# Performance work log

Measured on AMD Instinct MI355X. Metric: run time of the kernel, lower is better.

The kernel has to match this reference:

```python
import jax, jax.numpy as jnp
import numpy as np

B, T, S, N, C, H = 2, 16, 256, 32, 3072, 24
D = C // H  # 128 head_dim
EPS = 1e-6


def _layernorm(x):
    # LayerNorm, elementwise_affine=False, eps=1e-6
    mu = jnp.mean(x, axis=-1, keepdims=True)
    var = jnp.mean(jnp.square(x - mu), axis=-1, keepdims=True)
    return (x - mu) * jax.lax.rsqrt(var + EPS)


def _rmsnorm(x, w):
    # RMSNorm with learnable weight, computed in fp32 (matches x.float() path)
    ms = jnp.mean(jnp.square(x), axis=-1, keepdims=True)
    return x * jax.lax.rsqrt(ms + EPS) * w


def setup_inputs() -> dict:
    key = jax.random.key(0)
    ks = jax.random.split(key, 8)
    f = lambda k, sh: jax.random.normal(k, sh, dtype=jnp.float32)
    sc = 1.0 / np.sqrt(C)
    return {
        "x": f(ks[0], (B, T * S, C)),
        "motion_vec": f(ks[1], (B, T, N, C)),
        "motion_mask": jax.random.uniform(ks[2], (B, T * S), dtype=jnp.float32),
        "w_kv": f(ks[3], (2 * C, C)) * sc,
        "b_kv": jnp.zeros((2 * C,), jnp.float32),
        "w_q": f(ks[4], (C, C)) * sc,
        "b_q": jnp.zeros((C,), jnp.float32),
        "w_o": f(ks[5], (C, C)) * sc,
        "b_o": jnp.zeros((C,), jnp.float32),
        "q_norm_w": jnp.ones((D,), jnp.float32),
        "k_norm_w": jnp.ones((D,), jnp.float32),
    }


def reference(x, motion_vec, motion_mask, w_kv, b_kv, w_q, b_q, w_o, b_o,
              q_norm_w, k_norm_w):
    x_motion = _layernorm(motion_vec)            # [B,T,N,C]
    x_feat = _layernorm(x)                       # [B,T*S,C]

    kv = x_motion @ w_kv.T + b_kv                # [B,T,N,2C]
    kv = kv.reshape(B, T, N, 2, H, D)
    k, v = kv[:, :, :, 0], kv[:, :, :, 1]        # [B,T,N,H,D]

    q = (x_feat @ w_q.T + b_q).reshape(B, T, S, H, D)
    q = _rmsnorm(q, q_norm_w)
    k = _rmsnorm(k, k_norm_w)

    # frame-local cross-attention: queries = spatial tokens, keys = motion tokens
    scale = 1.0 / jnp.sqrt(jnp.float32(D))
    scores = jnp.einsum('btshd,btnhd->bthsn', q, k) * scale  # [B,T,H,S,N]
    probs = jax.nn.softmax(scores, axis=-1)
    attn = jnp.einsum('bthsn,btnhd->btshd', probs, v)        # [B,T,S,H,D]
    attn = attn.reshape(B, T * S, C)

    out = attn @ w_o.T + b_o                     # [B,T*S,C]
    return out * motion_mask[:, :, None]
```

## Files before the change

kernel.cpp:

```cpp
#include <hip/hip_runtime.h>
#include <math.h>

typedef unsigned short u16;
typedef unsigned int u32;
typedef short bf16x8 __attribute__((ext_vector_type(8)));
typedef float f32x4 __attribute__((ext_vector_type(4)));
typedef u16 u16x4 __attribute__((ext_vector_type(4)));
typedef u16 u16x8 __attribute__((ext_vector_type(8)));
typedef u32 u32x4 __attribute__((ext_vector_type(4)));

static __device__ __forceinline__ float b2f(u16 u) {
  union { u32 i; float f; } v; v.i = ((u32)u) << 16; return v.f;
}
static __device__ __forceinline__ u16 f2b(float f) {
  union { float f; u32 i; } v; v.f = f;
  u32 r = v.i + 0x7fffu + ((v.i >> 16) & 1u);
  return (u16)(r >> 16);
}
static __device__ __forceinline__ void cvt16(const float* src, u16* dst, int i) {
  f32x4 v = *(const f32x4*)(src + (size_t)i * 4);
  u16x4 w; w.x = f2b(v.x); w.y = f2b(v.y); w.z = f2b(v.z); w.w = f2b(v.w);
  *(u16x4*)(dst + (size_t)i * 4) = w;
}

static __device__ __forceinline__ void g2l16(const void* g, void* l) {
  typedef __attribute__((address_space(1))) const void gvoid;
  typedef __attribute__((address_space(3))) void lvoid;
  __builtin_amdgcn_global_load_lds((gvoid*)g, (lvoid*)l, 16, 0, 0);
}

__global__ __launch_bounds__(256)
void wcvt_kernel(const float* __restrict__ src, u16* __restrict__ dst, int n4)
{
  for (int i = blockIdx.x * 256 + threadIdx.x; i < n4; i += gridDim.x * 256)
    cvt16(src, dst, i);
}

__global__ __launch_bounds__(256)
void prep_kernel(const float* __restrict__ x, const float* __restrict__ mv,
                 u16* __restrict__ xf, u16* __restrict__ xm,
                 const float* __restrict__ wq, u16* __restrict__ wqs,
                 const float* __restrict__ wkv, u16* __restrict__ wkvs)
{
  const int b = blockIdx.x, tid = threadIdx.x;
  if (b >= 9216) {
    if (b < 10240) {
      const int n4 = 3072 * 3072 / 4;
      for (int i = (b - 9216) * 256 + tid; i < n4; i += 1024 * 256) cvt16(wq, wqs, i);
    } else {
      const int n4 = 6144 * 3072 / 4;
      for (int i = (b - 10240) * 256 + tid; i < n4; i += 1024 * 256) cvt16(wkv, wkvs, i);
    }
    return;
  }
  const float* src; u16* dst;
  if (b < 8192) { src = x + (size_t)b * 3072;          dst = xf + (size_t)b * 3072; }
  else          { src = mv + (size_t)(b - 8192) * 3072; dst = xm + (size_t)(b - 8192) * 3072; }

  f32x4 vals[3];
  #pragma unroll
  for (int i = 0; i < 3; ++i) vals[i] = *(const f32x4*)(src + tid * 4 + i * 1024);

  float s1 = 0.f, s2 = 0.f;
  #pragma unroll
  for (int i = 0; i < 3; ++i) {
    f32x4 v = vals[i];
    s1 += v.x + v.y + v.z + v.w;
    s2 += v.x * v.x + v.y * v.y + v.z * v.z + v.w * v.w;
  }
  #pragma unroll
  for (int o = 32; o > 0; o >>= 1) { s1 += __shfl_down(s1, o); s2 += __shfl_down(s2, o); }
  __shared__ float r1[4], r2[4];
  const int wv = tid >> 6, ln = tid & 63;
  if (ln == 0) { r1[wv] = s1; r2[wv] = s2; }
  __syncthreads();
  const float t1 = r1[0] + r1[1] + r1[2] + r1[3];
  const float t2 = r2[0] + r2[1] + r2[2] + r2[3];
  const float mu = t1 * (1.f / 3072.f);
  const float rs = rsqrtf(t2 * (1.f / 3072.f) - mu * mu + 1e-6f);
  #pragma unroll
  for (int i = 0; i < 3; ++i) {
    f32x4 v = vals[i]; u16x4 w;
    w.x = f2b((v.x - mu) * rs); w.y = f2b((v.y - mu) * rs);
    w.z = f2b((v.z - mu) * rs); w.w = f2b((v.w - mu) * rs);
    *(u16x4*)(dst + tid * 4 + i * 1024) = w;
  }
}

template<int EPI, typename TOUT>
__global__ __launch_bounds__(512, 1)
void gemm8p(const u16* __restrict__ A, const u16* __restrict__ Wb,
            const float* __restrict__ bias, const float* __restrict__ mask,
            TOUT* __restrict__ C, int M, int N, int K)
{
  __shared__ __align__(16) u16 L[65536];
  const int tid = threadIdx.x, wave = tid >> 6, lane = tid & 63;
  const int wr = wave >> 2, wc = wave & 3;
  const int lr = lane & 15, lg = lane >> 4;

  const int nwg = gridDim.x;
  const int bid = (blockIdx.x & 7) * (nwg >> 3) + (blockIdx.x >> 3);
  const int nbx = N >> 8;
  const int brow = (bid / nbx) << 8;
  const int bcol = (bid % nbx) << 8;

  const u16* gA = A + (size_t)brow * K;
  const u16* gB = Wb + (size_t)bcol * K;

  const int sr = tid >> 3;
  const int sc = 8 * ((tid & 7) ^ (sr & 7));
  const int ch0 = 8 * (lg ^ (lr & 7));
  const int ch1 = 8 * ((4 + lg) ^ (lr & 7));

  f32x4 acc[8][4] = {};

  auto SG = [&](int sel, int d, int h, int T) {
    const u16* g = (sel == 0 ? gA : gB) + (size_t)(h * 128 + sr) * K + T * 64 + sc;
    u16* l = &L[sel * 32768 + (d * 2 + h) * 8192 + tid * 8];
    g2l16(g, l);
    g2l16(g + (size_t)64 * K, l + 4096);
  };
  auto LDA = [&](int d, int mh, bf16x8 a[4][2]) {
    const u16* base = &L[(d * 2 + wr) * 8192 + mh * 4096 + lr * 64];
    #pragma unroll
    for (int mm = 0; mm < 4; ++mm) {
      a[mm][0] = *(const bf16x8*)&base[mm * 1024 + ch0];
      a[mm][1] = *(const bf16x8*)&base[mm * 1024 + ch1];
    }
  };
  auto LDB = [&](int d, int nh, bf16x8 b[2][2]) {
    const u16* base = &L[32768 + (d * 2 + (wc >> 1)) * 8192 + (wc & 1) * 4096 + nh * 2048 + lr * 64];
    #pragma unroll
    for (int nn = 0; nn < 2; ++nn) {
      b[nn][0] = *(const bf16x8*)&base[nn * 1024 + ch0];
      b[nn][1] = *(const bf16x8*)&base[nn * 1024 + ch1];
    }
  };

#define MM8P(mh, nh, a, b)                                                     \
  __builtin_amdgcn_s_setprio(1);                                               \
  _Pragma("unroll")                                                            \
  for (int mm = 0; mm < 4; ++mm)                                               \
    _Pragma("unroll")                                                          \
    for (int nn = 0; nn < 2; ++nn) {                                           \
      acc[(mh)*4+mm][(nh)*2+nn] = __builtin_amdgcn_mfma_f32_16x16x32_bf16(     \
          a[mm][0], b[nn][0], acc[(mh)*4+mm][(nh)*2+nn], 0, 0, 0);             \
      acc[(mh)*4+mm][(nh)*2+nn] = __builtin_amdgcn_mfma_f32_16x16x32_bf16(     \
          a[mm][1], b[nn][1], acc[(mh)*4+mm][(nh)*2+nn], 0, 0, 0);             \
    }                                                                          \
  __builtin_amdgcn_s_setprio(0);

#define BAR_PRE()                                                              \
  asm volatile("" ::: "memory");                                               \
  __builtin_amdgcn_s_barrier();                                                \
  asm volatile("s_waitcnt lgkmcnt(0)" ::: "memory");                           \
  __builtin_amdgcn_sched_barrier(0);

#define BAR_POST()                                                             \
  asm volatile("" ::: "memory");                                               \
  __builtin_amdgcn_s_barrier();                                                \
  __builtin_amdgcn_sched_barrier(0);

  SG(0, 0, 0, 0); SG(0, 0, 1, 0); SG(1, 0, 0, 0); SG(1, 0, 1, 0);
  SG(0, 1, 0, 1);
  asm volatile("s_waitcnt vmcnt(2)" ::: "memory");
  __builtin_amdgcn_s_barrier();
  __builtin_amdgcn_sched_barrier(0);

  const int NI = K >> 7;
  for (int i = 0; i < NI; ++i) {
    const int t = 2 * i;
    const bool pf = (i + 1) < NI;
    bf16x8 a[4][2], b[2][2];

    LDA(0, 0, a); LDB(0, 0, b);
    SG(0, 1, 1, t + 1);
    BAR_PRE(); MM8P(0, 0, a, b); BAR_POST();

    LDB(0, 1, b);
    SG(1, 1, 0, t + 1);
    BAR_PRE(); MM8P(0, 1, a, b); BAR_POST();

    LDA(0, 1, a);
    SG(1, 1, 1, t + 1);
    BAR_PRE(); MM8P(1, 1, a, b); BAR_POST();

    LDB(0, 0, b);
    if (pf) SG(0, 0, 0, t + 2);
    BAR_PRE(); MM8P(1, 0, a, b);
    if (pf) { asm volatile("s_waitcnt vmcnt(2)" ::: "memory"); }
    else    { asm volatile("s_waitcnt vmcnt(0)" ::: "memory"); }
    BAR_POST();

    LDA(1, 0, a); LDB(1, 0, b);
    if (pf) SG(0, 0, 1, t + 2);
    BAR_PRE(); MM8P(0, 0, a, b); BAR_POST();

    LDB(1, 1, b);
    if (pf) SG(1, 0, 0, t + 2);
    BAR_PRE(); MM8P(0, 1, a, b); BAR_POST();

    LDA(1, 1, a);
    if (pf) SG(1, 0, 1, t + 2);
    BAR_PRE(); MM8P(1, 1, a, b); BAR_POST();

    LDB(1, 0, b);
    if (pf) SG(0, 1, 0, t + 3);
    BAR_PRE(); MM8P(1, 0, a, b);
    if (pf) { asm volatile("s_waitcnt vmcnt(2)" ::: "memory"); }
    BAR_POST();
  }

#undef MM8P
#undef BAR_PRE
#undef BAR_POST

  #pragma unroll
  for (int m = 0; m < 8; ++m) {
    const int row = brow + wr * 128 + m * 16 + (lg << 2);
    #pragma unroll
    for (int n = 0; n < 4; ++n) {
      const int col = bcol + wc * 64 + n * 16 + lr;
      const float bv = bias[col];
      #pragma unroll
      for (int i = 0; i < 4; ++i) {
        float v = acc[m][n][i] + bv;
        if (EPI == 1) v *= mask[row + i];
        if constexpr (__is_same(TOUT, u16))
          C[(size_t)(row + i) * N + col] = f2b(v);
        else
          C[(size_t)(row + i) * N + col] = v;
      }
    }
  }
}

template<int EPI, typename TOUT>
__global__ __launch_bounds__(256, 2)
void gemm256(const u16* __restrict__ A, const u16* __restrict__ Wb,
             const float* __restrict__ bias, const float* __restrict__ mask,
             TOUT* __restrict__ C, int M, int N, int K)
{
  __shared__ __align__(16) u16 L[36864];
  const int tid = threadIdx.x, wave = tid >> 6, lane = tid & 63;

  const int nwg = gridDim.x;
  const int bid = (blockIdx.x & 7) * (nwg >> 3) + (blockIdx.x >> 3);
  const int nbx = N >> 7;
  const int brow = (bid / nbx) << 8;
  const int bcol = (bid % nbx) << 7;
  const int wr = wave >> 1, wc = wave & 1;

  const u16* gA = A + (size_t)brow * K;
  const u16* gB = Wb + (size_t)bcol * K;

  const int srow = tid >> 2;
  const int scol = 8 * ((lane & 3) ^ ((lane >> 3) & 3));
  const int rcoff = 8 * ((lane >> 4) ^ ((lane >> 1) & 3));

  f32x4 acc[8][4] = {};

  auto STAGE = [&](int b, int tk) {
    u16* bufA = &L[b * 12288];
    u16* bufB = bufA + 8192;
    const u16* srcA = gA + tk + scol;
    const u16* srcB = gB + tk + scol;
    #pragma unroll
    for (int j = 0; j < 4; ++j)
      g2l16(srcA + (size_t)(j * 64 + srow) * K, bufA + (j * 64 + wave * 16) * 32);
    #pragma unroll
    for (int j = 0; j < 2; ++j)
      g2l16(srcB + (size_t)(j * 64 + srow) * K, bufB + (j * 64 + wave * 16) * 32);
  };

  auto COMPUTE = [&](int b) {
    const u16* bufA = &L[b * 12288];
    const u16* bufB = bufA + 8192;
    bf16x8 af[8], bfv[4];
    #pragma unroll
    for (int m = 0; m < 8; ++m)
      af[m] = *(const bf16x8*)&bufA[(wr * 128 + m * 16 + (lane & 15)) * 32 + rcoff];
    #pragma unroll
    for (int n = 0; n < 4; ++n)
      bfv[n] = *(const bf16x8*)&bufB[(wc * 64 + n * 16 + (lane & 15)) * 32 + rcoff];
    __builtin_amdgcn_s_setprio(1);
    #pragma unroll
    for (int m = 0; m < 8; ++m)
      #pragma unroll
      for (int n = 0; n < 4; ++n)
        acc[m][n] = __builtin_amdgcn_mfma_f32_16x16x32_bf16(af[m], bfv[n], acc[m][n], 0, 0, 0);
    __builtin_amdgcn_s_setprio(0);
  };

  STAGE(0, 0);
  STAGE(1, 32);
  asm volatile("s_waitcnt vmcnt(6)" ::: "memory");
  __builtin_amdgcn_s_barrier();
  __builtin_amdgcn_sched_barrier(0);

  const int NT = K >> 5;
  int cur = 0;
  for (int t = 0; t < NT; ++t) {
    const bool pf = (t + 2) < NT;
    if (pf) {
      int nb = cur + 2; if (nb >= 3) nb -= 3;
      STAGE(nb, (t + 2) << 5);
    }
    COMPUTE(cur);
    if (pf) asm volatile("s_waitcnt vmcnt(6)" ::: "memory");
    else    asm volatile("s_waitcnt vmcnt(0)" ::: "memory");
    __builtin_amdgcn_s_barrier();
    __builtin_amdgcn_sched_barrier(0);
    if (++cur == 3) cur = 0;
  }

  #pragma unroll
  for (int m = 0; m < 8; ++m) {
    const int row = brow + wr * 128 + m * 16 + ((lane >> 4) << 2);
    #pragma unroll
    for (int n = 0; n < 4; ++n) {
      const int col = bcol + wc * 64 + n * 16 + (lane & 15);
      const float bv = bias[col];
      #pragma unroll
      for (int i = 0; i < 4; ++i) {
        float v = acc[m][n][i] + bv;
        if (EPI == 1) v *= mask[row + i];
        if constexpr (__is_same(TOUT, u16))
          C[(size_t)(row + i) * N + col] = f2b(v);
        else
          C[(size_t)(row + i) * N + col] = v;
      }
    }
  }
}

template<int EPI, typename TOUT>
__global__ __launch_bounds__(256)
void gemm_mixed(const u16* __restrict__ A, const float* __restrict__ W,
                const float* __restrict__ bias, const float* __restrict__ mask,
                TOUT* __restrict__ C, int M, int N, int K)
{
  __shared__ __align__(16) u16 lA[4096];
  __shared__ __align__(16) u16 lB[4096];
  const int tid = threadIdx.x, wave = tid >> 6, lane = tid & 63;
  const int nbx = N >> 7;
  const int brow = (blockIdx.x / nbx) << 7;
  const int bcol = (blockIdx.x % nbx) << 7;
  const int wr = wave >> 1, wc = wave & 1;

  f32x4 acc[4][4] = {};
  const u16* gA = A + (size_t)brow * K;
  const float* gB = W + (size_t)bcol * K;
  const int br = tid >> 1, bk0 = (tid & 1) << 4;
  const float* bsrc0 = gB + (size_t)br * K + bk0;
  u16* bdst = &lB[br * 32 + bk0];

  for (int tk = 0; tk < K; tk += 32) {
    #pragma unroll
    for (int j = 0; j < 2; ++j) {
      const int c = j * 256 + wave * 64 + lane;
      const int r = c >> 2, k8 = (c & 3) << 3;
      g2l16(gA + (size_t)r * K + tk + k8, (char*)lA + (size_t)(j * 256 + wave * 64) * 16);
    }
    {
      const float* src = bsrc0 + tk;
      #pragma unroll
      for (int j = 0; j < 4; ++j) {
        f32x4 v = *(const f32x4*)(src + 4 * j);
        u16x4 w; w.x = f2b(v.x); w.y = f2b(v.y); w.z = f2b(v.z); w.w = f2b(v.w);
        *(u16x4*)(bdst + 4 * j) = w;
      }
    }
    __syncthreads();

    bf16x8 af[4], bfr[4];
    #pragma unroll
    for (int m = 0; m < 4; ++m)
      af[m] = *(const bf16x8*)&lA[(wr * 64 + m * 16 + (lane & 15)) * 32 + ((lane >> 4) << 3)];
    #pragma unroll
    for (int n = 0; n < 4; ++n)
      bfr[n] = *(const bf16x8*)&lB[(wc * 64 + n * 16 + (lane & 15)) * 32 + ((lane >> 4) << 3)];
    #pragma unroll
    for (int m = 0; m < 4; ++m)
      #pragma unroll
      for (int n = 0; n < 4; ++n)
        acc[m][n] = __builtin_amdgcn_mfma_f32_16x16x32_bf16(af[m], bfr[n], acc[m][n], 0, 0, 0);
    __syncthreads();
  }

  #pragma unroll
  for (int m = 0; m < 4; ++m) {
    const int row = brow + wr * 64 + m * 16 + ((lane >> 4) << 2);
    #pragma unroll
    for (int n = 0; n < 4; ++n) {
      const int col = bcol + wc * 64 + n * 16 + (lane & 15);
      const float bv = bias[col];
      #pragma unroll
      for (int i = 0; i < 4; ++i) {
        float v = acc[m][n][i] + bv;
        if (EPI == 1) v *= mask[row + i];
        if constexpr (__is_same(TOUT, u16))
          C[(size_t)(row + i) * N + col] = f2b(v);
        else
          C[(size_t)(row + i) * N + col] = v;
      }
    }
  }
}

__global__ __launch_bounds__(256)
void attn_wcvt(const u16* __restrict__ qb, const u16* __restrict__ kvb,
               const float* __restrict__ qw, const float* __restrict__ kw,
               u16* __restrict__ attnb,
               const float* __restrict__ wo, u16* __restrict__ wos)
{
  __shared__ __align__(16) u16 Kn[32 * 136];
  __shared__ __align__(16) u16 Vt[128 * 40];
  __shared__ __align__(16) u16 Pl[256 * 40];
  __shared__ __align__(16) u16 Ol[4][16 * 136];
  const int tid = threadIdx.x;
  if (blockIdx.x >= 768) {
    const int n4 = 3072 * 3072 / 4;
    for (int i = (blockIdx.x - 768) * 256 + tid; i < n4; i += 1024 * 256)
      cvt16(wo, wos, i);
    return;
  }
  const int wave = tid >> 6, lane = tid & 63;
  const int h = blockIdx.x % 24;
  const int bt = blockIdx.x / 24;

  {
    const int n = tid >> 3, sub = tid & 7;
    const size_t base = (size_t)(bt * 32 + n) * 6144 + (size_t)h * 128;
    const u16* kp = kvb + base + sub * 16;
    u16x8 k0 = *(const u16x8*)kp;
    u16x8 k1 = *(const u16x8*)(kp + 8);
    float kv_[16]; float ss = 0.f;
    #pragma unroll
    for (int j = 0; j < 8; ++j) { kv_[j] = b2f(k0[j]); kv_[8 + j] = b2f(k1[j]); }
    #pragma unroll
    for (int j = 0; j < 16; ++j) ss += kv_[j] * kv_[j];
    ss += __shfl_xor(ss, 1); ss += __shfl_xor(ss, 2); ss += __shfl_xor(ss, 4);
    const float krs = rsqrtf(ss * (1.f / 128.f) + 1e-6f);
    u16x8 w0, w1;
    #pragma unroll
    for (int j = 0; j < 8; ++j) {
      const int d = sub * 16 + j;
      w0[j] = f2b(kv_[j] * krs * kw[d] * qw[d]);
      w1[j] = f2b(kv_[8 + j] * krs * kw[d + 8] * qw[d + 8]);
    }
    *(u16x8*)&Kn[n * 136 + sub * 16] = w0;
    *(u16x8*)&Kn[n * 136 + sub * 16 + 8] = w1;
  }
  {
    const int k = tid >> 3, dc = (tid & 7) * 16;
    const u16* vp = kvb + (size_t)(bt * 32 + k) * 6144 + (size_t)h * 128 + 3072 + dc;
    u16x8 v0 = *(const u16x8*)vp;
    u16x8 v1 = *(const u16x8*)(vp + 8);
    #pragma unroll
    for (int j = 0; j < 8; ++j) {
      Vt[(dc + j) * 40 + k] = v0[j];
      Vt[(dc + 8 + j) * 40 + k] = v1[j];
    }
  }
  __syncthreads();

  const int q0 = wave * 64;
  const int lr = lane & 15, lg = lane >> 4;

  for (int m = 0; m < 4; ++m) {
    const int qrow = q0 + m * 16 + lr;
    const u16* qp = qb + (size_t)(bt * 256 + qrow) * 3072 + (size_t)h * 128 + lg * 8;
    bf16x8 qf[4];
    #pragma unroll
    for (int k = 0; k < 4; ++k) qf[k] = *(const bf16x8*)(qp + k * 32);
    float ss = 0.f;
    #pragma unroll
    for (int k = 0; k < 4; ++k)
      #pragma unroll
      for (int j = 0; j < 8; ++j) { const float f = b2f((u16)qf[k][j]); ss += f * f; }
    ss += __shfl_xor(ss, 16); ss += __shfl_xor(ss, 32);
    const float qsc = rsqrtf(ss * (1.f / 128.f) + 1e-6f) * 0.08838834764831845f;
    #pragma unroll
    for (int k = 0; k < 4; ++k)
      #pragma unroll
      for (int j = 0; j < 8; ++j)
        qf[k][j] = (short)f2b(b2f((u16)qf[k][j]) * qsc);

    f32x4 s0 = {0.f, 0.f, 0.f, 0.f}, s1 = {0.f, 0.f, 0.f, 0.f};
    #pragma unroll
    for (int k = 0; k < 4; ++k) {
      bf16x8 kb0 = *(const bf16x8*)&Kn[(lr) * 136 + k * 32 + lg * 8];
      bf16x8 kb1 = *(const bf16x8*)&Kn[(16 + lr) * 136 + k * 32 + lg * 8];
      s0 = __builtin_amdgcn_mfma_f32_16x16x32_bf16(qf[k], kb0, s0, 0, 0, 0);
      s1 = __builtin_amdgcn_mfma_f32_16x16x32_bf16(qf[k], kb1, s1, 0, 0, 0);
    }

    float mx[4], sm[4], e0[4], e1[4];
    #pragma unroll
    for (int i = 0; i < 4; ++i) mx[i] = fmaxf(s0[i], s1[i]);
    #pragma unroll
    for (int o = 1; o <= 8; o <<= 1)
      #pragma unroll
      for (int i = 0; i < 4; ++i) mx[i] = fmaxf(mx[i], __shfl_xor(mx[i], o));
    #pragma unroll
    for (int i = 0; i < 4; ++i) {
      e0[i] = __expf(s0[i] - mx[i]);
      e1[i] = __expf(s1[i] - mx[i]);
      sm[i] = e0[i] + e1[i];
    }
    #pragma unroll
    for (int o = 1; o <= 8; o <<= 1)
      #pragma unroll
      for (int i = 0; i < 4; ++i) sm[i] += __shfl_xor(sm[i], o);
    #pragma unroll
    for (int i = 0; i < 4; ++i) {
      const float inv = 1.f / sm[i];
      const int pr = (q0 + m * 16 + lg * 4 + i) * 40;
      Pl[pr + lr] = f2b(e0[i] * inv);
      Pl[pr + 16 + lr] = f2b(e1[i] * inv);
    }
    asm volatile("s_waitcnt lgkmcnt(0)" ::: "memory");
    __builtin_amdgcn_sched_barrier(0);

    bf16x8 pf = *(const bf16x8*)&Pl[(q0 + m * 16 + lr) * 40 + lg * 8];
    f32x4 o_[8];
    #pragma unroll
    for (int n = 0; n < 8; ++n) {
      bf16x8 vb = *(const bf16x8*)&Vt[(n * 16 + lr) * 40 + lg * 8];
      o_[n] = __builtin_amdgcn_mfma_f32_16x16x32_bf16(
                pf, vb, (f32x4){0.f, 0.f, 0.f, 0.f}, 0, 0, 0);
    }

    u16* ow = &Ol[wave][0];
    #pragma unroll
    for (int n = 0; n < 8; ++n)
      #pragma unroll
      for (int i = 0; i < 4; ++i)
        ow[(lg * 4 + i) * 136 + n * 16 + lr] = f2b(o_[n][i]);
    asm volatile("s_waitcnt lgkmcnt(0)" ::: "memory");
    __builtin_amdgcn_sched_barrier(0);
    const int r = lane >> 2, cc = (lane & 3) * 32;
    u16* gout = attnb + (size_t)(bt * 256 + q0 + m * 16 + r) * 3072 + (size_t)h * 128 + cc;
    #pragma unroll
    for (int c = 0; c < 4; ++c)
      *(u16x8*)(gout + c * 8) = *(const u16x8*)&ow[r * 136 + cc + c * 8];
    asm volatile("s_waitcnt lgkmcnt(0)" ::: "memory");
    __builtin_amdgcn_sched_barrier(0);
  }
}

extern "C" void kernel_launch(void* const* d_in, const int* in_sizes, int n_in,
                              void* d_out, int out_size, void* d_ws, size_t ws_size,
                              hipStream_t stream) {
  const float* x    = (const float*)d_in[0];
  const float* mv   = (const float*)d_in[1];
  const float* mask = (const float*)d_in[2];
  const float* wkv  = (const float*)d_in[3];
  const float* bkv  = (const float*)d_in[4];
  const float* wq   = (const float*)d_in[5];
  const float* bq   = (const float*)d_in[6];
  const float* wo   = (const float*)d_in[7];
  const float* bo   = (const float*)d_in[8];
  const float* qnw  = (const float*)d_in[9];
  const float* knw  = (const float*)d_in[10];
  float* out = (float*)d_out;

  char* ws = (char*)d_ws;

  if (ws_size >= 176160768u) {
    u16* wqs  = (u16*)(ws);
    u16* wkvs = (u16*)(ws + 18874368);
    u16* xf   = (u16*)(ws + 56623104);
    u16* xm   = (u16*)(ws + 106954752);
    u16* qbuf = (u16*)(ws + 113246208);
    u16* kvb  = (u16*)(ws + 163577856);
    u16* wos  = wqs;

    prep_kernel<<<11264, 256, 0, stream>>>(x, mv, xf, xm, wq, wqs, wkv, wkvs);
    gemm8p<0, u16><<<384, 512, 0, stream>>>(xf, wqs, bq, nullptr, qbuf, 8192, 3072, 3072);
    gemm256<0, u16><<<192, 256, 0, stream>>>(xm, wkvs, bkv, nullptr, kvb, 1024, 6144, 3072);
    attn_wcvt<<<1792, 256, 0, stream>>>(qbuf, kvb, qnw, knw, xf, wo, wos);
    gemm8p<1, float><<<384, 512, 0, stream>>>(xf, wos, bo, mask, out, 8192, 3072, 3072);
  } else if (ws_size >= 157286400u) {
    u16* xf    = (u16*)(ws);
    u16* xm    = (u16*)(ws + 50331648);
    u16* qbuf  = (u16*)(ws + 56623104);
    u16* kvb   = (u16*)(ws + 106954752);
    u16* wslab = (u16*)(ws + 119537664);

    prep_kernel<<<9216, 256, 0, stream>>>(x, mv, xf, xm, wq, wslab, wkv, wslab);
    wcvt_kernel<<<2048, 256, 0, stream>>>(wq, wslab, 3072 * 3072 / 4);
    gemm8p<0, u16><<<384, 512, 0, stream>>>(xf, wslab, bq, nullptr, qbuf, 8192, 3072, 3072);
    wcvt_kernel<<<2048, 256, 0, stream>>>(wkv, wslab, 6144 * 3072 / 4);
    gemm256<0, u16><<<192, 256, 0, stream>>>(xm, wslab, bkv, nullptr, kvb, 1024, 6144, 3072);
    attn_wcvt<<<768, 256, 0, stream>>>(qbuf, kvb, qnw, knw, xf, wo, wslab);
    wcvt_kernel<<<2048, 256, 0, stream>>>(wo, wslab, 3072 * 3072 / 4);
    gemm8p<1, float><<<384, 512, 0, stream>>>(xf, wslab, bo, mask, out, 8192, 3072, 3072);
  } else {
    u16* xf   = (u16*)(ws);
    u16* xm   = (u16*)(ws + 50331648);
    u16* qbuf = (u16*)(ws + 56623104);
    u16* kvb  = (u16*)(ws + 106954752);

    prep_kernel<<<9216, 256, 0, stream>>>(x, mv, xf, xm, wq, xf, wkv, xf);
    gemm_mixed<0, u16><<<1536, 256, 0, stream>>>(xf, wq, bq, nullptr, qbuf, 8192, 3072, 3072);
    gemm_mixed<0, u16><<<384, 256, 0, stream>>>(xm, wkv, bkv, nullptr, kvb, 1024, 6144, 3072);
    attn_wcvt<<<768, 256, 0, stream>>>(qbuf, kvb, qnw, knw, xf, wo, xf);
    gemm_mixed<1, float><<<1536, 256, 0, stream>>>(xf, wo, bo, mask, out, 8192, 3072, 3072);
  }
}
```

Baseline: 496.7 us.

## Add 128x192-tile GEMM for output projection and deepen gemm8p prefetch grouping

Adds a new gemm192 kernel with 128x192 tiles, a triple-buffered LDS pipeline and two blocks per CU. It replaces gemm8p for the final output projection, where 1024 blocks should fill the CUs better than 384. Separately, the gemm8p main loop now issues its global-to-LDS stages in pairs, with vmcnt waits raised to match. That runs more loads ahead but groups them at fewer points in the schedule.

```diff
diff --git a/kernel.cpp b/kernel.cpp
--- a/kernel.cpp
+++ b/kernel.cpp
@@ -162,8 +162,8 @@
   __builtin_amdgcn_sched_barrier(0);
 
   SG(0, 0, 0, 0); SG(0, 0, 1, 0); SG(1, 0, 0, 0); SG(1, 0, 1, 0);
-  SG(0, 1, 0, 1);
-  asm volatile("s_waitcnt vmcnt(2)" ::: "memory");
+  SG(0, 1, 0, 1); SG(0, 1, 1, 1);
+  asm volatile("s_waitcnt vmcnt(4)" ::: "memory");
   __builtin_amdgcn_s_barrier();
   __builtin_amdgcn_sched_barrier(0);
 
@@ -174,40 +174,36 @@
     bf16x8 a[4][2], b[2][2];
 
     LDA(0, 0, a); LDB(0, 0, b);
-    SG(0, 1, 1, t + 1);
+    SG(1, 1, 0, t + 1); SG(1, 1, 1, t + 1);
     BAR_PRE(); MM8P(0, 0, a, b); BAR_POST();
 
     LDB(0, 1, b);
-    SG(1, 1, 0, t + 1);
     BAR_PRE(); MM8P(0, 1, a, b); BAR_POST();
 
     LDA(0, 1, a);
-    SG(1, 1, 1, t + 1);
     BAR_PRE(); MM8P(1, 1, a, b); BAR_POST();
 
     LDB(0, 0, b);
-    if (pf) SG(0, 0, 0, t + 2);
+    if (pf) { SG(0, 0, 0, t + 2); SG(0, 0, 1, t + 2); }
     BAR_PRE(); MM8P(1, 0, a, b);
-    if (pf) { asm volatile("s_waitcnt vmcnt(2)" ::: "memory"); }
+    if (pf) { asm volatile("s_waitcnt vmcnt(4)" ::: "memory"); }
     else    { asm volatile("s_waitcnt vmcnt(0)" ::: "memory"); }
     BAR_POST();
 
     LDA(1, 0, a); LDB(1, 0, b);
-    if (pf) SG(0, 0, 1, t + 2);
+    if (pf) { SG(1, 0, 0, t + 2); SG(1, 0, 1, t + 2); }
     BAR_PRE(); MM8P(0, 0, a, b); BAR_POST();
 
     LDB(1, 1, b);
-    if (pf) SG(1, 0, 0, t + 2);
     BAR_PRE(); MM8P(0, 1, a, b); BAR_POST();
 
     LDA(1, 1, a);
-    if (pf) SG(1, 0, 1, t + 2);
     BAR_PRE(); MM8P(1, 1, a, b); BAR_POST();
 
     LDB(1, 0, b);
-    if (pf) SG(0, 1, 0, t + 3);
+    if (pf) { SG(0, 1, 0, t + 3); SG(0, 1, 1, t + 3); }
     BAR_PRE(); MM8P(1, 0, a, b);
-    if (pf) { asm volatile("s_waitcnt vmcnt(2)" ::: "memory"); }
+    if (pf) { asm volatile("s_waitcnt vmcnt(4)" ::: "memory"); }
     BAR_POST();
   }
 
@@ -320,6 +316,105 @@
     #pragma unroll
     for (int n = 0; n < 4; ++n) {
       const int col = bcol + wc * 64 + n * 16 + (lane & 15);
+      const float bv = bias[col];
+      #pragma unroll
+      for (int i = 0; i < 4; ++i) {
+        float v = acc[m][n][i] + bv;
+        if (EPI == 1) v *= mask[row + i];
+        if constexpr (__is_same(TOUT, u16))
+          C[(size_t)(row + i) * N + col] = f2b(v);
+        else
+          C[(size_t)(row + i) * N + col] = v;
+      }
+    }
+  }
+}
+
+template<int EPI, typename TOUT>
+__global__ __launch_bounds__(256, 2)
+void gemm192(const u16* __restrict__ A, const u16* __restrict__ Wb,
+             const float* __restrict__ bias, const float* __restrict__ mask,
+             TOUT* __restrict__ C, int M, int N, int K)
+{
+  __shared__ __align__(16) u16 L[30720];
+  const int tid = threadIdx.x, wave = tid >> 6, lane = tid & 63;
+  const int nwg = gridDim.x;
+  const int tb = (blockIdx.x & 7) * (nwg >> 3) + (blockIdx.x >> 3);
+  const int nbx = N / 192;
+  const int brow = (tb / nbx) << 7;
+  const int bcol = (tb % nbx) * 192;
+  const int wr = wave >> 1, wc = wave & 1;
+
+  const u16* gA = A + (size_t)brow * K;
+  const u16* gB = Wb + (size_t)bcol * K;
+
+  const int srow = tid >> 2;
+  const int scol = 8 * ((lane & 3) ^ ((lane >> 3) & 3));
+  const int rcoff = 8 * ((lane >> 4) ^ ((lane >> 1) & 3));
+  const int lr = lane & 15;
+
+  f32x4 acc[4][6] = {};
+
+  auto STAGE = [&](int b, int tk) {
+    u16* bufA = &L[b * 10240];
+    u16* bufB = bufA + 4096;
+    const u16* srcA = gA + tk + scol;
+    const u16* srcB = gB + tk + scol;
+    #pragma unroll
+    for (int j = 0; j < 2; ++j)
+      g2l16(srcA + (size_t)(j * 64 + srow) * K, bufA + (j * 64 + wave * 16) * 32);
+    #pragma unroll
+    for (int j = 0; j < 3; ++j)
+      g2l16(srcB + (size_t)(j * 64 + srow) * K, bufB + (j * 64 + wave * 16) * 32);
+  };
+
+  auto COMPUTE = [&](int b) {
+    const u16* bufA = &L[b * 10240];
+    const u16* bufB = bufA + 4096;
+    bf16x8 af[4], bfv[6];
+    #pragma unroll
+    for (int m = 0; m < 4; ++m)
+      af[m] = *(const bf16x8*)&bufA[(wr * 64 + m * 16 + lr) * 32 + rcoff];
+    #pragma unroll
+    for (int n = 0; n < 6; ++n)
+      bfv[n] = *(const bf16x8*)&bufB[(wc * 96 + n * 16 + lr) * 32 + rcoff];
+    __builtin_amdgcn_s_setprio(1);
+    #pragma unroll
+    for (int m = 0; m < 4; ++m)
+      #pragma unroll
+      for (int n = 0; n < 6; ++n)
+        acc[m][n] = __builtin_amdgcn_mfma_f32_16x16x32_bf16(af[m], bfv[n], acc[m][n], 0, 0, 0);
+    __builtin_amdgcn_s_setprio(0);
+  };
+
+  STAGE(0, 0);
+  STAGE(1, 32);
+  asm volatile("s_waitcnt vmcnt(5)" ::: "memory");
+  __builtin_amdgcn_s_barrier();
+  __builtin_amdgcn_sched_barrier(0);
+
+  const int NT = K >> 5;
+  int cur = 0;
+  for (int t = 0; t < NT; ++t) {
+    const bool pf = (t + 2) < NT;
+    if (pf) {
+      int nb = cur + 2; if (nb >= 3) nb -= 3;
+      STAGE(nb, (t + 2) << 5);
+    }
+    COMPUTE(cur);
+    if (pf) asm volatile("s_waitcnt vmcnt(5)" ::: "memory");
+    else    asm volatile("s_waitcnt vmcnt(0)" ::: "memory");
+    __builtin_amdgcn_s_barrier();
+    __builtin_amdgcn_sched_barrier(0);
+    if (++cur == 3) cur = 0;
+  }
+
+  #pragma unroll
+  for (int m = 0; m < 4; ++m) {
+    const int row = brow + wr * 64 + m * 16 + ((lane >> 4) << 2);
+    #pragma unroll
+    for (int n = 0; n < 6; ++n) {
+      const int col = bcol + wc * 96 + n * 16 + lr;
       const float bv = bias[col];
       #pragma unroll
       for (int i = 0; i < 4; ++i) {
@@ -581,7 +676,7 @@
     gemm8p<0, u16><<<384, 512, 0, stream>>>(xf, wqs, bq, nullptr, qbuf, 8192, 3072, 3072);
     gemm256<0, u16><<<192, 256, 0, stream>>>(xm, wkvs, bkv, nullptr, kvb, 1024, 6144, 3072);
     attn_wcvt<<<1792, 256, 0, stream>>>(qbuf, kvb, qnw, knw, xf, wo, wos);
-    gemm8p<1, float><<<384, 512, 0, stream>>>(xf, wos, bo, mask, out, 8192, 3072, 3072);
+    gemm192<1, float><<<1024, 256, 0, stream>>>(xf, wos, bo, mask, out, 8192, 3072, 3072);
   } else if (ws_size >= 157286400u) {
     u16* xf    = (u16*)(ws);
     u16* xm    = (u16*)(ws + 50331648);
@@ -596,7 +691,7 @@
     gemm256<0, u16><<<192, 256, 0, stream>>>(xm, wslab, bkv, nullptr, kvb, 1024, 6144, 3072);
     attn_wcvt<<<768, 256, 0, stream>>>(qbuf, kvb, qnw, knw, xf, wo, wslab);
     wcvt_kernel<<<2048, 256, 0, stream>>>(wo, wslab, 3072 * 3072 / 4);
-    gemm8p<1, float><<<384, 512, 0, stream>>>(xf, wslab, bo, mask, out, 8192, 3072, 3072);
+    gemm192<1, float><<<1024, 256, 0, stream>>>(xf, wslab, bo, mask, out, 8192, 3072, 3072);
   } else {
     u16* xf   = (u16*)(ws);
     u16* xm   = (u16*)(ws + 50331648);
```

New measurement: 494.1 us. No clear change (-0.5%).
